# Performance work log

Hardware: AMD Instinct MI355X
Metric: run time of the kernel (lower is better)

## Reference

```python
import jax, jax.numpy as jnp
import numpy as np

ALPHA = 0.2          # LeakyReLU negative slope
NEG_INF = -9e15      # matches torch's -9000000000000000.0 mask value


def _gat_layer(x, adj_mask, W, a1, a2, concat):
    """One GraphAttentionLayerBatch (eval mode, dropout off).

    The original builds a_input = [h_i || h_j] of shape [B,N,N,2F] and dots
    with a = [a1; a2]; that is mathematically the separable score
    a1.h_i + a2.h_j, which we compute directly without the O(N^2*2F) tensor.
    """
    h = jnp.einsum('bnf,fo->bno', x, W)            # [B, N, F_out]
    f1 = jnp.einsum('bno,o->bn', h, a1)            # a1 . h_i
    f2 = jnp.einsum('bno,o->bn', h, a2)            # a2 . h_j
    e = jax.nn.leaky_relu(f1[:, :, None] + f2[:, None, :], negative_slope=ALPHA)
    e = jnp.where(adj_mask, e, NEG_INF)            # [B, N, N]
    att = jax.nn.softmax(e, axis=2)
    h_prime = jnp.einsum('bnm,bmo->bno', att, h)   # [B, N, F_out]
    return jax.nn.elu(h_prime) if concat else h_prime


def setup_inputs() -> dict:
    key = jax.random.key(0)
    ks = jax.random.split(key, 9)
    B, N, nfeat, nhid, nclass, H = 32, 512, 128, 64, 16, 8
    x = jax.random.normal(ks[0], (B, N, nfeat), dtype=jnp.float32)
    adj = jax.random.randint(ks[1], (B, N, N), 0, 2, dtype=jnp.int32)
    W_heads = jax.random.normal(ks[2], (H, nfeat, nhid), dtype=jnp.float32) * 0.1
    a1_heads = jax.random.normal(ks[3], (H, nhid), dtype=jnp.float32) * 0.1
    a2_heads = jax.random.normal(ks[4], (H, nhid), dtype=jnp.float32) * 0.1
    W_out = jax.random.normal(ks[5], (nhid * H, nclass), dtype=jnp.float32) * 0.05
    a1_out = jax.random.normal(ks[6], (nclass,), dtype=jnp.float32) * 0.1
    a2_out = jax.random.normal(ks[7], (nclass,), dtype=jnp.float32) * 0.1
    return {"x": x, "adj": adj, "W_heads": W_heads, "a1_heads": a1_heads,
            "a2_heads": a2_heads, "W_out": W_out, "a1_out": a1_out,
            "a2_out": a2_out}


def reference(x, adj, W_heads, a1_heads, a2_heads, W_out, a1_out, a2_out):
    mask = adj > 0  # [B, N, N]
    # multi-head attention layers (concat=True)
    heads = jax.vmap(lambda W, a1, a2: _gat_layer(x, mask, W, a1, a2, True))(
        W_heads, a1_heads, a2_heads)              # [H, B, N, nhid]
    H, B, N, F = heads.shape
    x_cat = jnp.transpose(heads, (1, 2, 0, 3)).reshape(B, N, H * F)
    # output attention layer (concat=False)
    return _gat_layer(x_cat, mask, W_out, a1_out, a2_out, False)
```

## Files before the change

kernel.cpp:

```cpp
#include <hip/hip_runtime.h>

#define GB 32
#define GN 512
#define GFIN 128
#define GFH 64
#define GH 8
#define GC 16

typedef short short8 __attribute__((ext_vector_type(8)));
typedef float f32x4 __attribute__((ext_vector_type(4)));
typedef _Float16 h2 __attribute__((ext_vector_type(2)));
typedef _Float16 half8 __attribute__((ext_vector_type(8)));

__device__ __forceinline__ ushort f2h(float f) {
  _Float16 h = (_Float16)f;
  return __builtin_bit_cast(ushort, h);
}
__device__ __forceinline__ h2 cvt_pk(float a, float b) {
  return __builtin_bit_cast(h2, __builtin_amdgcn_cvt_pkrtz(a, b));
}
__device__ __forceinline__ unsigned pkh2(float a, float b) {
  return __builtin_bit_cast(unsigned, __builtin_amdgcn_cvt_pkrtz(a, b));
}
__device__ __forceinline__ short8 ones8() {
  short8 o;
#pragma unroll
  for (int i = 0; i < 8; ++i) o[i] = (short)0x3C00;
  return o;
}
__device__ __forceinline__ float fdiv_fast(float a, float b) {
  return a * __builtin_amdgcn_rcpf(b);
}
__device__ __forceinline__ f32x4 mfma_h(short8 a, short8 b, f32x4 c) {
  return __builtin_amdgcn_mfma_f32_16x16x32_f16(
      __builtin_bit_cast(half8, a), __builtin_bit_cast(half8, b), c, 0, 0, 0);
}

__device__ __forceinline__ uint4 score8(unsigned E1u, unsigned e1u,
                                        const h2* E2h, const h2* e2h,
                                        unsigned mb) {
  h2 E1h = __builtin_bit_cast(h2, E1u);
  h2 e1h = __builtin_bit_cast(h2, e1u);
  unsigned lo = (((mb & 0xFu) * 0x00204081u) & 0x01010101u) * 0xFFu;
  unsigned hi = (((mb >> 4) * 0x00204081u) & 0x01010101u) * 0xFFu;
  unsigned m0 = __builtin_amdgcn_perm(lo, lo, 0x01010000u);
  unsigned m1 = __builtin_amdgcn_perm(lo, lo, 0x03030202u);
  unsigned m2 = __builtin_amdgcn_perm(hi, hi, 0x01010000u);
  unsigned m3 = __builtin_amdgcn_perm(hi, hi, 0x03030202u);
  uint4 u;
  u.x = __builtin_bit_cast(unsigned,
          __builtin_elementwise_max(E1h * E2h[0], e1h * e2h[0])) & m0;
  u.y = __builtin_bit_cast(unsigned,
          __builtin_elementwise_max(E1h * E2h[1], e1h * e2h[1])) & m1;
  u.z = __builtin_bit_cast(unsigned,
          __builtin_elementwise_max(E1h * E2h[2], e1h * e2h[2])) & m2;
  u.w = __builtin_bit_cast(unsigned,
          __builtin_elementwise_max(E1h * E2h[3], e1h * e2h[3])) & m3;
  return u;
}

__global__ __launch_bounds__(256) void k_pack_gemm1(
    const int* __restrict__ adj, unsigned* __restrict__ mw,
    const float* __restrict__ xg, const float* __restrict__ Wg,
    const float* __restrict__ a1g, const float* __restrict__ a2g,
    ushort* __restrict__ VTg, float* __restrict__ f1g, float* __restrict__ f2g,
    const float* __restrict__ Wog, ushort* __restrict__ WoT) {
  __shared__ ushort Wt[64][136];
  __shared__ ushort xl[64][136];
  int blk = blockIdx.x;
  int tid = threadIdx.x;

  if (blk == 6144) {
    for (int i = tid; i < 512 * GC; i += 256) {
      int k = i & 511, cc = i >> 9;
      WoT[cc * 512 + k] = f2h(Wog[(size_t)k * GC + cc]);
    }
    return;
  }
  if (blk < 4096) {
    int pblk = blk;
    int4 v0 = *(const int4*)&adj[(size_t)pblk * 2048 + tid * 4];
    int4 v1 = *(const int4*)&adj[(size_t)pblk * 2048 + 1024 + tid * 4];
    int sh = 4 * (tid & 7);
    unsigned b0 = ((v0.x > 0) ? 1u : 0u) | ((v0.y > 0) ? 2u : 0u) |
                  ((v0.z > 0) ? 4u : 0u) | ((v0.w > 0) ? 8u : 0u);
    unsigned b1 = ((v1.x > 0) ? 1u : 0u) | ((v1.y > 0) ? 2u : 0u) |
                  ((v1.z > 0) ? 4u : 0u) | ((v1.w > 0) ? 8u : 0u);
    unsigned m0 = b0 << sh, m1 = b1 << sh;
    m0 |= __shfl_xor(m0, 1); m1 |= __shfl_xor(m1, 1);
    m0 |= __shfl_xor(m0, 2); m1 |= __shfl_xor(m1, 2);
    m0 |= __shfl_xor(m0, 4); m1 |= __shfl_xor(m1, 4);
    if ((tid & 7) == 0) {
      mw[pblk * 64 + (tid >> 3)] = m0;
      mw[pblk * 64 + 32 + (tid >> 3)] = m1;
    }
    return;
  }

  int gblk = blk - 4096;
  int bh = gblk >> 3, rs8 = gblk & 7;
  int b = bh >> 3, h = bh & 7;
  int r0 = rs8 * 64;
  int lane = tid & 63, w = tid >> 6;
  int c = lane & 15, q = lane >> 4;

  const float* Wh = Wg + (size_t)h * GFIN * GFH;
  for (int u4 = tid; u4 < GFIN * GFH / 4; u4 += 256) {
    int i0 = u4 * 4;
    int f = i0 >> 6, j0 = i0 & 63;
    float4 wv = *(const float4*)&Wh[i0];
    Wt[j0 + 0][f] = f2h(wv.x);
    Wt[j0 + 1][f] = f2h(wv.y);
    Wt[j0 + 2][f] = f2h(wv.z);
    Wt[j0 + 3][f] = f2h(wv.w);
  }
  const float* xb = xg + ((size_t)b * GN + r0) * GFIN;
  for (int u = tid; u < 64 * 32; u += 256) {
    int row = u >> 5, c4 = u & 31;
    float4 xf = *(const float4*)&xb[(size_t)row * GFIN + c4 * 4];
    uint2 us;
    us.x = pkh2(xf.x, xf.y);
    us.y = pkh2(xf.z, xf.w);
    *(uint2*)&xl[row][c4 * 4] = us;
  }
  __syncthreads();

  short8 Bf[4][4];
#pragma unroll
  for (int cb = 0; cb < 4; ++cb)
#pragma unroll
    for (int kk = 0; kk < 4; ++kk)
      Bf[cb][kk] = *(const short8*)&Wt[cb * 16 + c][kk * 32 + q * 8];

  float a1v[4], a2v[4];
#pragma unroll
  for (int cb = 0; cb < 4; ++cb) {
    a1v[cb] = a1g[h * 64 + cb * 16 + c];
    a2v[cb] = a2g[h * 64 + cb * 16 + c];
  }

  f32x4 acc[4];
#pragma unroll
  for (int cb = 0; cb < 4; ++cb) acc[cb] = (f32x4){0.f, 0.f, 0.f, 0.f};

#pragma unroll
  for (int kk = 0; kk < 4; ++kk) {
    short8 A = *(const short8*)&xl[w * 16 + c][kk * 32 + q * 8];
#pragma unroll
    for (int cb = 0; cb < 4; ++cb)
      acc[cb] = mfma_h(A, Bf[cb][kk], acc[cb]);
  }

  ushort* VT = VTg + (size_t)bh * GN * GFH;
  float* f1o = f1g + (size_t)bh * GN;
  float* f2o = f2g + (size_t)bh * GN;
  int rowb = r0 + w * 16 + q * 4;
  float v1[4] = {0.f, 0.f, 0.f, 0.f}, v2[4] = {0.f, 0.f, 0.f, 0.f};
#pragma unroll
  for (int cb = 0; cb < 4; ++cb) {
    f32x4 a = acc[cb];
    uint2 vs;
    vs.x = pkh2(a[0], a[1]);
    vs.y = pkh2(a[2], a[3]);
    *(uint2*)&VT[(size_t)(cb * 16 + c) * GN + rowb] = vs;
#pragma unroll
    for (int i = 0; i < 4; ++i) {
      v1[i] += a[i] * a1v[cb];
      v2[i] += a[i] * a2v[cb];
    }
  }
#pragma unroll
  for (int i = 0; i < 4; ++i) {
#pragma unroll
    for (int off = 1; off < 16; off <<= 1) {
      v1[i] += __shfl_xor(v1[i], off);
      v2[i] += __shfl_xor(v2[i], off);
    }
    if (c == 0) { f1o[rowb + i] = v1[i]; f2o[rowb + i] = v2[i]; }
  }
}

__global__ __launch_bounds__(256, 4) void k_attn1(
    const ushort* __restrict__ VTg, const unsigned* __restrict__ mwg,
    const float* __restrict__ f1g, const float* __restrict__ f2g,
    ushort* __restrict__ xcb) {
  __shared__ ushort P[2][16][520];
  int blk = blockIdx.x;
  int bh = blk & 255, slice = blk >> 8;
  int b = bh >> 3, h = bh & 7;
  int r0 = slice * 128;
  int tid = threadIdx.x, lane = tid & 63, w = tid >> 6;
  int c = lane & 15, q = lane >> 4;

  const unsigned* mwb = mwg + (size_t)b * GN * 16;
  const float* f1w = f1g + (size_t)bh * GN;
  const float* f2w = f2g + (size_t)bh * GN;

  float4 fa = *(const float4*)&f2w[lane * 8];
  float4 fb = *(const float4*)&f2w[lane * 8 + 4];
  h2 E2h[4], e2h[4];
  {
    float f2v[8] = {fa.x, fa.y, fa.z, fa.w, fb.x, fb.y, fb.z, fb.w};
#pragma unroll
    for (int j = 0; j < 4; ++j) {
      E2h[j] = cvt_pk(__expf(f2v[2 * j]), __expf(f2v[2 * j + 1]));
      e2h[j] = cvt_pk(__expf(0.2f * f2v[2 * j]), __expf(0.2f * f2v[2 * j + 1]));
    }
  }
  float f1a = f1w[r0 + lane];
  float f1b = f1w[r0 + 64 + lane];
  unsigned E1pk0 = pkh2(__expf(f1a - 4.f), __expf(f1a - 4.f));
  unsigned e1pk0 = pkh2(__expf(0.2f * f1a - 4.f), __expf(0.2f * f1a - 4.f));
  unsigned E1pk1 = pkh2(__expf(f1b - 4.f), __expf(f1b - 4.f));
  unsigned e1pk1 = pkh2(__expf(0.2f * f1b - 4.f), __expf(0.2f * f1b - 4.f));

  const ushort* VT = VTg + (size_t)bh * GN * GFH + (size_t)(w * 16 + c) * GN + q * 8;
  short8 Bf[16];
#pragma unroll
  for (int kk = 0; kk < 16; ++kk) Bf[kk] = *(const short8*)&VT[kk * 32];
  const short8 ONES = ones8();

  unsigned mn[4];
#pragma unroll
  for (int ri = 0; ri < 4; ++ri)
    mn[ri] = mwb[(size_t)(r0 + w + 4 * ri) * 16 + (lane >> 2)];
#pragma unroll
  for (int ri = 0; ri < 4; ++ri) {
    unsigned E1u = (unsigned)__builtin_amdgcn_readlane((int)E1pk0, w + 4 * ri);
    unsigned e1u = (unsigned)__builtin_amdgcn_readlane((int)e1pk0, w + 4 * ri);
    unsigned mb = (mn[ri] >> (8 * (lane & 3))) & 0xffu;
    uint4 u = score8(E1u, e1u, E2h, e2h, mb);
    *(uint4*)&P[0][w + 4 * ri][lane * 8] = u;
  }
#pragma unroll
  for (int ri = 0; ri < 4; ++ri)
    mn[ri] = mwb[(size_t)(r0 + 16 + w + 4 * ri) * 16 + (lane >> 2)];
  __syncthreads();

#pragma unroll
  for (int t = 0; t < 8; ++t) {
    int tb = r0 + t * 16;
    const ushort (*Pc)[520] = P[t & 1];

    f32x4 acc = (f32x4){0.f, 0.f, 0.f, 0.f};
    f32x4 aL = (f32x4){0.f, 0.f, 0.f, 0.f};
#pragma unroll
    for (int kk = 0; kk < 16; ++kk) {
      short8 A = *(const short8*)&Pc[c][kk * 32 + q * 8];
      acc = mfma_h(A, Bf[kk], acc);
      aL  = mfma_h(A, ONES, aL);
    }

    if (t < 7) {
      int rowbase = (t + 1) * 16;
#pragma unroll
      for (int ri = 0; ri < 4; ++ri) {
        int row = rowbase + w + 4 * ri;
        unsigned E1u, e1u;
        if (row < 64) {
          E1u = (unsigned)__builtin_amdgcn_readlane((int)E1pk0, row);
          e1u = (unsigned)__builtin_amdgcn_readlane((int)e1pk0, row);
        } else {
          E1u = (unsigned)__builtin_amdgcn_readlane((int)E1pk1, row - 64);
          e1u = (unsigned)__builtin_amdgcn_readlane((int)e1pk1, row - 64);
        }
        unsigned mb = (mn[ri] >> (8 * (lane & 3))) & 0xffu;
        uint4 u = score8(E1u, e1u, E2h, e2h, mb);
        *(uint4*)&P[(t + 1) & 1][w + 4 * ri][lane * 8] = u;
      }
      if (t < 6) {
#pragma unroll
        for (int ri = 0; ri < 4; ++ri)
          mn[ri] = mwb[(size_t)(tb + 32 + w + 4 * ri) * 16 + (lane >> 2)];
      }
    }

#pragma unroll
    for (int i = 0; i < 4; ++i) {
      int row = tb + q * 4 + i;
      float v = fdiv_fast(acc[i], fmaxf(aL[i], 1e-30f));
      v = v > 0.f ? v : __expf(v) - 1.f;
      xcb[((size_t)(b * GN + row)) * 512 + h * 64 + w * 16 + c] = f2h(v);
    }
    __syncthreads();
  }
}

__global__ __launch_bounds__(256) void k_gemm2(
    const ushort* __restrict__ xcb, const ushort* __restrict__ WoT,
    const float* __restrict__ a1o, const float* __restrict__ a2o,
    ushort* __restrict__ hTg, float* __restrict__ f1bg,
    float* __restrict__ f2bg) {
  int vb = blockIdx.x;
  int b = vb >> 3, r0 = (vb & 7) * 64;
  int tid = threadIdx.x, lane = tid & 63, w = tid >> 6;
  int c = lane & 15, q = lane >> 4;

  short8 Bf[16];
#pragma unroll
  for (int kk = 0; kk < 16; ++kk)
    Bf[kk] = *(const short8*)&WoT[(size_t)c * 512 + kk * 32 + q * 8];

  const ushort* xrow = xcb + ((size_t)(b * GN + r0 + w * 16 + c)) * 512 + q * 8;
  f32x4 acc = (f32x4){0.f, 0.f, 0.f, 0.f};
#pragma unroll
  for (int kk = 0; kk < 16; ++kk) {
    short8 A = *(const short8*)&xrow[kk * 32];
    acc = mfma_h(A, Bf[kk], acc);
  }

  float a1v = a1o[c], a2v = a2o[c];
  int rowb = r0 + w * 16 + q * 4;
  uint2 vs;
  vs.x = pkh2(acc[0], acc[1]);
  vs.y = pkh2(acc[2], acc[3]);
  *(uint2*)&hTg[((size_t)b * GC + c) * 512 + rowb] = vs;
#pragma unroll
  for (int i = 0; i < 4; ++i) {
    float v1 = acc[i] * a1v, v2 = acc[i] * a2v;
#pragma unroll
    for (int off = 1; off < 16; off <<= 1) {
      v1 += __shfl_xor(v1, off);
      v2 += __shfl_xor(v2, off);
    }
    if (c == 0) {
      f1bg[(size_t)b * GN + rowb + i] = v1;
      f2bg[(size_t)b * GN + rowb + i] = v2;
    }
  }
}

__global__ __launch_bounds__(256) void k_attn2(
    const ushort* __restrict__ hTg, const unsigned* __restrict__ mwg,
    const float* __restrict__ f1g, const float* __restrict__ f2g,
    float* __restrict__ outg) {
  __shared__ ushort P[32][520];
  __shared__ float pacc[2][64][8];
  int vb = blockIdx.x;
  int b = vb >> 4, r0 = (vb & 15) * 32;
  int tid = threadIdx.x, lane = tid & 63, w = tid >> 6;
  int c = lane & 15, q = lane >> 4;
  const short8 ONES = ones8();

  const unsigned* mwb = mwg + (size_t)b * GN * 16;
  const float* f1w = f1g + (size_t)b * GN;
  const float* f2w = f2g + (size_t)b * GN;

  float4 fa = *(const float4*)&f2w[lane * 8];
  float4 fb = *(const float4*)&f2w[lane * 8 + 4];
  h2 E2h[4], e2h[4];
  {
    float f2v[8] = {fa.x, fa.y, fa.z, fa.w, fb.x, fb.y, fb.z, fb.w};
#pragma unroll
    for (int j = 0; j < 4; ++j) {
      E2h[j] = cvt_pk(__expf(f2v[2 * j]), __expf(f2v[2 * j + 1]));
      e2h[j] = cvt_pk(__expf(0.2f * f2v[2 * j]), __expf(0.2f * f2v[2 * j + 1]));
    }
  }
  float f1v = 0.f;
  if (lane < 8) f1v = f1w[r0 + w * 8 + lane];
  float E1f = __expf(f1v - 4.f), e1f = __expf(0.2f * f1v - 4.f);
  unsigned E1pk = pkh2(E1f, E1f);
  unsigned e1pk = pkh2(e1f, e1f);

  unsigned mword[8];
#pragma unroll
  for (int ri = 0; ri < 8; ++ri)
    mword[ri] = mwb[(size_t)(r0 + w * 8 + ri) * 16 + (lane >> 2)];
#pragma unroll
  for (int ri = 0; ri < 8; ++ri) {
    unsigned E1u = (unsigned)__builtin_amdgcn_readlane((int)E1pk, ri);
    unsigned e1u = (unsigned)__builtin_amdgcn_readlane((int)e1pk, ri);
    unsigned mb = (mword[ri] >> (8 * (lane & 3))) & 0xffu;
    uint4 u = score8(E1u, e1u, E2h, e2h, mb);
    *(uint4*)&P[w * 8 + ri][lane * 8] = u;
  }
  __syncthreads();

  int tile = w & 1, kh = w >> 1;
  short8 Bf[8];
#pragma unroll
  for (int kk = 0; kk < 8; ++kk)
    Bf[kk] = *(const short8*)&hTg[((size_t)b * GC + c) * 512 +
                                  (kh * 8 + kk) * 32 + q * 8];
  f32x4 acc = (f32x4){0.f, 0.f, 0.f, 0.f};
  f32x4 aL = (f32x4){0.f, 0.f, 0.f, 0.f};
#pragma unroll
  for (int kk = 0; kk < 8; ++kk) {
    short8 A = *(const short8*)&P[tile * 16 + c][(kh * 8 + kk) * 32 + q * 8];
    acc = mfma_h(A, Bf[kk], acc);
    aL  = mfma_h(A, ONES, aL);
  }
  if (kh == 1) {
#pragma unroll
    for (int i = 0; i < 4; ++i) {
      pacc[tile][lane][i] = acc[i];
      pacc[tile][lane][4 + i] = aL[i];
    }
  }
  __syncthreads();
  if (kh == 0) {
#pragma unroll
    for (int i = 0; i < 4; ++i) {
      acc[i] += pacc[tile][lane][i];
      aL[i] += pacc[tile][lane][4 + i];
    }
#pragma unroll
    for (int i = 0; i < 4; ++i) {
      int row = r0 + tile * 16 + q * 4 + i;
      outg[((size_t)(b * GN + row)) * GC + c] =
          fdiv_fast(acc[i], fmaxf(aL[i], 1e-30f));
    }
  }
}

extern "C" void kernel_launch(void* const* d_in, const int* in_sizes, int n_in,
                              void* d_out, int out_size, void* d_ws, size_t ws_size,
                              hipStream_t stream) {
  (void)in_sizes; (void)n_in; (void)out_size;
  const float* x   = (const float*)d_in[0];
  const int*   adj = (const int*)d_in[1];
  const float* Whd = (const float*)d_in[2];
  const float* a1h = (const float*)d_in[3];
  const float* a2h = (const float*)d_in[4];
  const float* Wo  = (const float*)d_in[5];
  const float* a1o = (const float*)d_in[6];
  const float* a2o = (const float*)d_in[7];

  size_t off = 0;
  char* base = (char*)d_ws;
  unsigned* mw = (unsigned*)(base + off); off += (size_t)GB * GN * 16 * 4;
  ushort* VT   = (ushort*)(base + off);   off += (size_t)GB * GH * GN * GFH * 2;
  ushort* xcb  = (ushort*)(base + off);   off += (size_t)GB * GN * 512 * 2;
  ushort* WoT  = (ushort*)(base + off);   off += (size_t)GC * 512 * 2;
  ushort* hT   = (ushort*)(base + off);   off += (size_t)GB * GC * GN * 2;
  float* f1    = (float*)(base + off);    off += (size_t)GB * GH * GN * 4;
  float* f2    = (float*)(base + off);    off += (size_t)GB * GH * GN * 4;
  float* f1b   = (float*)(base + off);    off += (size_t)GB * GN * 4;
  float* f2b   = (float*)(base + off);    off += (size_t)GB * GN * 4;

  if (ws_size < off) return;

  hipLaunchKernelGGL(k_pack_gemm1, dim3(6145), dim3(256), 0, stream,
                     adj, mw, x, Whd, a1h, a2h, VT, f1, f2, Wo, WoT);
  hipLaunchKernelGGL(k_attn1, dim3(1024), dim3(256), 0, stream,
                     VT, mw, f1, f2, xcb);
  hipLaunchKernelGGL(k_gemm2, dim3(256), dim3(256), 0, stream,
                     xcb, WoT, a1o, a2o, hT, f1b, f2b);
  hipLaunchKernelGGL(k_attn2, dim3(512), dim3(256), 0, stream,
                     hT, mw, f1b, f2b, (float*)d_out);
}
```

Baseline: 144.7 us.

## Compute attention scores in-register per MFMA fragment instead of via shared P tile

Each wave now builds its MFMA A-operand scores directly in registers from a small shared table of exp(f2) values and per-row mask words. This drops the double-buffered shared P score tile and the per-iteration block barriers. The cost is redundant work: every wave recomputes the same scores, because the four waves share rows but differ in output columns. The 4-waves launch-bounds hint is also removed.

```diff
diff --git a/kernel.cpp b/kernel.cpp
--- a/kernel.cpp
+++ b/kernel.cpp
@@ -180,11 +180,11 @@
   }
 }
 
-__global__ __launch_bounds__(256, 4) void k_attn1(
+__global__ __launch_bounds__(256) void k_attn1(
     const ushort* __restrict__ VTg, const unsigned* __restrict__ mwg,
     const float* __restrict__ f1g, const float* __restrict__ f2g,
     ushort* __restrict__ xcb) {
-  __shared__ ushort P[2][16][520];
+  __shared__ h2 etab[2][64][4];
   int blk = blockIdx.x;
   int bh = blk & 255, slice = blk >> 8;
   int b = bh >> 3, h = bh & 7;
@@ -196,83 +196,52 @@
   const float* f1w = f1g + (size_t)bh * GN;
   const float* f2w = f2g + (size_t)bh * GN;
 
-  float4 fa = *(const float4*)&f2w[lane * 8];
-  float4 fb = *(const float4*)&f2w[lane * 8 + 4];
-  h2 E2h[4], e2h[4];
   {
-    float f2v[8] = {fa.x, fa.y, fa.z, fa.w, fb.x, fb.y, fb.z, fb.w};
-#pragma unroll
-    for (int j = 0; j < 4; ++j) {
-      E2h[j] = cvt_pk(__expf(f2v[2 * j]), __expf(f2v[2 * j + 1]));
-      e2h[j] = cvt_pk(__expf(0.2f * f2v[2 * j]), __expf(0.2f * f2v[2 * j + 1]));
-    }
-  }
-  float f1a = f1w[r0 + lane];
-  float f1b = f1w[r0 + 64 + lane];
-  unsigned E1pk0 = pkh2(__expf(f1a - 4.f), __expf(f1a - 4.f));
-  unsigned e1pk0 = pkh2(__expf(0.2f * f1a - 4.f), __expf(0.2f * f1a - 4.f));
-  unsigned E1pk1 = pkh2(__expf(f1b - 4.f), __expf(f1b - 4.f));
-  unsigned e1pk1 = pkh2(__expf(0.2f * f1b - 4.f), __expf(0.2f * f1b - 4.f));
+    int col0 = tid * 2;
+    float a = f2w[col0], bb = f2w[col0 + 1];
+    etab[0][col0 >> 3][(col0 >> 1) & 3] = cvt_pk(__expf(a), __expf(bb));
+    etab[1][col0 >> 3][(col0 >> 1) & 3] =
+        cvt_pk(__expf(0.2f * a), __expf(0.2f * bb));
+  }
 
   const ushort* VT = VTg + (size_t)bh * GN * GFH + (size_t)(w * 16 + c) * GN + q * 8;
   short8 Bf[16];
 #pragma unroll
   for (int kk = 0; kk < 16; ++kk) Bf[kk] = *(const short8*)&VT[kk * 32];
   const short8 ONES = ones8();
-
-  unsigned mn[4];
-#pragma unroll
-  for (int ri = 0; ri < 4; ++ri)
-    mn[ri] = mwb[(size_t)(r0 + w + 4 * ri) * 16 + (lane >> 2)];
-#pragma unroll
-  for (int ri = 0; ri < 4; ++ri) {
-    unsigned E1u = (unsigned)__builtin_amdgcn_readlane((int)E1pk0, w + 4 * ri);
-    unsigned e1u = (unsigned)__builtin_amdgcn_readlane((int)e1pk0, w + 4 * ri);
-    unsigned mb = (mn[ri] >> (8 * (lane & 3))) & 0xffu;
-    uint4 u = score8(E1u, e1u, E2h, e2h, mb);
-    *(uint4*)&P[0][w + 4 * ri][lane * 8] = u;
-  }
-#pragma unroll
-  for (int ri = 0; ri < 4; ++ri)
-    mn[ri] = mwb[(size_t)(r0 + 16 + w + 4 * ri) * 16 + (lane >> 2)];
   __syncthreads();
 
+  ushort* xo = xcb + ((size_t)b * GN) * 512 + h * 64 + w * 16 + c;
 #pragma unroll
   for (int t = 0; t < 8; ++t) {
     int tb = r0 + t * 16;
-    const ushort (*Pc)[520] = P[t & 1];
+    int mrow = tb + c;
+    float f1v = f1w[mrow];
+    unsigned E1u = pkh2(__expf(f1v - 4.f), __expf(f1v - 4.f));
+    unsigned e1u = pkh2(__expf(0.2f * f1v - 4.f), __expf(0.2f * f1v - 4.f));
+    uint4 mA = *(const uint4*)&mwb[(size_t)mrow * 16 + 0];
+    uint4 mB = *(const uint4*)&mwb[(size_t)mrow * 16 + 4];
+    uint4 mC = *(const uint4*)&mwb[(size_t)mrow * 16 + 8];
+    uint4 mD = *(const uint4*)&mwb[(size_t)mrow * 16 + 12];
+    unsigned mn[16] = {mA.x, mA.y, mA.z, mA.w, mB.x, mB.y, mB.z, mB.w,
+                       mC.x, mC.y, mC.z, mC.w, mD.x, mD.y, mD.z, mD.w};
 
     f32x4 acc = (f32x4){0.f, 0.f, 0.f, 0.f};
     f32x4 aL = (f32x4){0.f, 0.f, 0.f, 0.f};
 #pragma unroll
     for (int kk = 0; kk < 16; ++kk) {
-      short8 A = *(const short8*)&Pc[c][kk * 32 + q * 8];
+      int g = kk * 4 + q;
+      uint4 ue = *(const uint4*)&etab[0][g][0];
+      uint4 uf = *(const uint4*)&etab[1][g][0];
+      h2 E2l[4] = {__builtin_bit_cast(h2, ue.x), __builtin_bit_cast(h2, ue.y),
+                   __builtin_bit_cast(h2, ue.z), __builtin_bit_cast(h2, ue.w)};
+      h2 e2l[4] = {__builtin_bit_cast(h2, uf.x), __builtin_bit_cast(h2, uf.y),
+                   __builtin_bit_cast(h2, uf.z), __builtin_bit_cast(h2, uf.w)};
+      unsigned mb = (mn[kk] >> (8 * q)) & 0xffu;
+      uint4 u = score8(E1u, e1u, E2l, e2l, mb);
+      short8 A = __builtin_bit_cast(short8, u);
       acc = mfma_h(A, Bf[kk], acc);
       aL  = mfma_h(A, ONES, aL);
-    }
-
-    if (t < 7) {
-      int rowbase = (t + 1) * 16;
-#pragma unroll
-      for (int ri = 0; ri < 4; ++ri) {
-        int row = rowbase + w + 4 * ri;
-        unsigned E1u, e1u;
-        if (row < 64) {
-          E1u = (unsigned)__builtin_amdgcn_readlane((int)E1pk0, row);
-          e1u = (unsigned)__builtin_amdgcn_readlane((int)e1pk0, row);
-        } else {
-          E1u = (unsigned)__builtin_amdgcn_readlane((int)E1pk1, row - 64);
-          e1u = (unsigned)__builtin_amdgcn_readlane((int)e1pk1, row - 64);
-        }
-        unsigned mb = (mn[ri] >> (8 * (lane & 3))) & 0xffu;
-        uint4 u = score8(E1u, e1u, E2h, e2h, mb);
-        *(uint4*)&P[(t + 1) & 1][w + 4 * ri][lane * 8] = u;
-      }
-      if (t < 6) {
-#pragma unroll
-        for (int ri = 0; ri < 4; ++ri)
-          mn[ri] = mwb[(size_t)(tb + 32 + w + 4 * ri) * 16 + (lane >> 2)];
-      }
     }
 
 #pragma unroll
@@ -280,9 +249,8 @@
       int row = tb + q * 4 + i;
       float v = fdiv_fast(acc[i], fmaxf(aL[i], 1e-30f));
       v = v > 0.f ? v : __expf(v) - 1.f;
-      xcb[((size_t)(b * GN + row)) * 512 + h * 64 + w * 16 + c] = f2h(v);
-    }
-    __syncthreads();
+      xo[(size_t)row * 512] = f2h(v);
+    }
   }
 }
 
```

Result: slower. 220.3 us (+52.3%).
